# Kernel optimization log

Hardware: AMD Instinct MI355X
Metric: run time of the kernel (lower is better)

Reference implementation:

```python
import jax, jax.numpy as jnp
import numpy as np

B, N, M, C, K, K1 = 2, 2048, 2048, 512, 16, 8
NN_MARGIN = 1.0
H1, H2 = 64, 128  # Discriminator MLP widths


def _pairwise_distance(x, y):
    # x: (B,C,N), y: (B,C,M) -> squared euclidean distances (B,N,M)
    xx = jnp.sum(x * x, axis=1)[:, :, None]
    yy = jnp.sum(y * y, axis=1)[:, None, :]
    return xx - 2.0 * jnp.einsum('bcn,bcm->bnm', x, y) + yy


def _discriminator(x, y, W1, b1, W2, b2, W3, b3):
    # x, y: (B,N,k,3) neighborhood difference tensors -> per-point weights (B,1,N)
    f = jnp.concatenate([x, y], axis=-1)                       # (B,N,k,6)
    h = jax.nn.relu(jnp.einsum('bnkc,dc->bnkd', f, W1) + b1)
    h = jax.nn.relu(jnp.einsum('bnkd,ed->bnke', h, W2) + b2)
    s = (jnp.einsum('bnke,oe->bnko', h, W3) + b3)[..., 0]      # (B,N,k)
    s = jnp.max(s, axis=2)                                     # max over neighbors
    return jax.nn.softmax(s, axis=1)[:, None, :]               # (B,1,N)


def _rigid(src, corr, weight):
    # weighted Kabsch/Procrustes. src, corr: (B,3,N), weight: (B,1,N)
    w = weight / jnp.sum(weight, axis=2, keepdims=True)
    cs = jnp.sum(src * w, axis=2, keepdims=True)
    ct = jnp.sum(corr * w, axis=2, keepdims=True)
    H = jnp.einsum('bin,bjn->bij', (src - cs) * w, corr - ct)
    U, S, Vt = jnp.linalg.svd(H)
    V = jnp.swapaxes(Vt, 1, 2)
    det = jnp.linalg.det(jnp.einsum('bij,bkj->bik', V, U))     # det(V U^T)
    scale = jnp.stack([jnp.ones_like(det), jnp.ones_like(det), det], axis=-1)[:, None, :]
    R = jnp.einsum('bij,bkj->bik', V * scale, U)
    t = ct - jnp.einsum('bij,bjn->bin', R, cs)
    return R, t


def _gather_pts(x_t, idx):
    # x_t: (B,N,3), idx: (B,N,K) -> (B,N,K,3)
    return jax.vmap(lambda xb, ib: xb[ib])(x_t, idx)


def _forward(src, tgt, src_embedding, tgt_embedding, src_knn, tgt_knn,
             W1, b1, W2, b2, W3, b3, src_idx, src_idx1, idx2, k, i, k1):
    Bs, _, Np = src.shape
    Mp = tgt.shape[2]
    dist = _pairwise_distance(src_embedding, tgt_embedding)    # (B,N,M)
    scores = jax.nn.softmax(-dist, axis=2)
    # rows of scores gathered at each source point's k1 neighbors: (B,N,k1,M)
    knn_scores = jax.vmap(lambda sb, ib: sb[ib])(scores, src_idx1)
    # equivalent to summing result_view[:,:,1:,:,1:] over axes 2 and 4:
    T = jnp.sum(knn_scores[:, :, 1:, :], axis=2)               # (B,N,M)
    S = jax.vmap(lambda Tb, ib: jnp.sum(Tb[:, ib[:, 1:]], axis=-1))(T, idx2)  # (B,N,M)
    src_knn_scores = NN_MARGIN - S / (k1 - 1)
    refined = jnp.exp(src_knn_scores) * dist
    rmm = jax.nn.softmax(-refined, axis=2)                     # refined matching map
    src_corr = jnp.einsum('bcm,bnm->bcn', tgt, rmm)            # (B,3,N)
    corr_t = jnp.swapaxes(src_corr, 1, 2)                      # (B,N,3)
    src_knn_corr = _gather_pts(corr_t, src_idx)                # (B,N,K,3)
    knn_distance = corr_t[:, :, None, :] - src_knn_corr
    src_t = jnp.swapaxes(src, 1, 2)
    src_knn_distance = src_t[:, :, None, :] - src_knn
    weight = _discriminator(knn_distance, src_knn_distance, W1, b1, W2, b2, W3, b3)
    R, t = _rigid(src, src_corr, weight)
    key_num = Np // 2
    if key_num < 900:
        key_num = key_num * 2
    _, topi = jax.lax.top_k(weight[:, 0, :], key_num)          # (B,key)
    gidx = jnp.broadcast_to(topi[:, None, :], (Bs, 3, key_num))
    src_keypoints = jnp.take_along_axis(src, gidx, axis=2)
    tgt_keypoints = jnp.take_along_axis(src_corr, gidx, axis=2)
    idx_tgt_corr = jnp.argmax(rmm, axis=-1)                    # (B,N)
    sel = jnp.take_along_axis(idx_tgt_corr, topi, axis=1)      # (B,key)
    onehot = jax.nn.one_hot(sel, Mp, dtype=rmm.dtype).reshape(Bs * key_num, Mp)
    pred = jax.vmap(lambda rb, ib: rb[ib])(rmm, topi).reshape(Bs * key_num, Mp)
    loss_scl = jnp.mean(jnp.sum(-jnp.log(pred + 1e-15) * onehot, axis=1))
    tgt_keypoints_knn = jnp.transpose(
        jax.vmap(lambda kd, ib: kd[ib])(knn_distance, topi), (0, 3, 1, 2))  # (B,3,key,K)
    tvec = t[:, :, 0]
    src_transformed = jnp.einsum('bij,bjn->bin', R, src) + tvec[:, :, None]
    st_t = jnp.swapaxes(src_transformed, 1, 2)
    knn_distance2 = st_t[:, :, None, :] - _gather_pts(st_t, src_idx)
    src_keypoints_knn = jnp.transpose(
        jax.vmap(lambda kd, ib: kd[ib])(knn_distance2, topi), (0, 3, 1, 2))
    return (R, tvec, src_keypoints, tgt_keypoints, src_keypoints_knn,
            tgt_keypoints_knn, loss_scl)


def setup_inputs() -> dict:
    key = jax.random.key(0)
    ks = jax.random.split(key, 14)
    src = jax.random.normal(ks[0], (B, 3, N), jnp.float32)
    tgt = jax.random.normal(ks[1], (B, 3, M), jnp.float32)
    src_embedding = jax.random.normal(ks[2], (B, C, N), jnp.float32) * 0.1
    tgt_embedding = jax.random.normal(ks[3], (B, C, M), jnp.float32) * 0.1
    src_idx = jax.random.randint(ks[4], (B, N, K), 0, N, jnp.int32)
    src_idx1 = jax.random.randint(ks[5], (B, N, K1), 0, N, jnp.int32)
    src_idx1 = src_idx1.at[:, :, 0].set(jnp.arange(N, dtype=jnp.int32)[None, :])
    idx2 = jax.random.randint(ks[6], (B, M, K1), 0, M, jnp.int32)
    idx2 = idx2.at[:, :, 0].set(jnp.arange(M, dtype=jnp.int32)[None, :])
    src_knn = _gather_pts(jnp.swapaxes(src, 1, 2), src_idx)    # (B,N,K,3)
    tgt_knn = jax.random.normal(ks[7], (B, M, K, 3), jnp.float32)  # unused by forward
    W1 = jax.random.normal(ks[8], (H1, 6), jnp.float32) * 0.1
    b1 = jnp.zeros((H1,), jnp.float32)
    W2 = jax.random.normal(ks[9], (H2, H1), jnp.float32) * 0.1
    b2 = jnp.zeros((H2,), jnp.float32)
    W3 = jax.random.normal(ks[10], (1, H2), jnp.float32) * 0.1
    b3 = jnp.zeros((1,), jnp.float32)
    return {"src": src, "tgt": tgt, "src_embedding": src_embedding,
            "tgt_embedding": tgt_embedding, "src_knn": src_knn, "tgt_knn": tgt_knn,
            "W1": W1, "b1": b1, "W2": W2, "b2": b2, "W3": W3, "b3": b3,
            "src_idx": src_idx, "src_idx1": src_idx1, "idx2": idx2,
            "k": K, "i": 1, "k1": K1}


def reference(src, tgt, src_embedding, tgt_embedding, src_knn, tgt_knn,
              W1, b1, W2, b2, W3, b3, src_idx, src_idx1, idx2, k, i, k1):
    return _forward(src, tgt, src_embedding, tgt_embedding, src_knn, tgt_knn,
                    W1, b1, W2, b2, W3, b3, src_idx, src_idx1, idx2, k, i, k1)
```

## Files before the change

### kernel.cpp

```cpp
#include <hip/hip_runtime.h>
#include <stdint.h>

typedef unsigned short u16;

#define BB 2
#define NN 2048
#define MM 2048
#define CC 512
#define KK 16
#define KK1 8
#define KEY 1024

typedef __attribute__((ext_vector_type(8))) short bf16x8;
typedef __attribute__((ext_vector_type(4))) float f32x4;

__device__ __forceinline__ float b2f(u16 u){ return __uint_as_float(((uint32_t)u) << 16); }
__device__ __forceinline__ u16 f2b(float f){
  uint32_t x = __float_as_uint(f);
  uint32_t r = x + 0x7FFFu + ((x >> 16) & 1u);
  return (u16)(r >> 16);
}
__device__ __forceinline__ float sane(float v){ return (fabsf(v) < 1e30f) ? v : 1e30f; }

__device__ __forceinline__ void gload_lds16(const u16* g, u16* l){
  __builtin_amdgcn_global_load_lds((const __attribute__((address_space(1))) uint32_t*)g,
                                   (__attribute__((address_space(3))) uint32_t*)l, 16, 0, 0);
}

__device__ __forceinline__ float blockRed(float v, float* red, int t, int op){
  red[t] = v; __syncthreads();
  #pragma unroll
  for (int s = 128; s > 0; s >>= 1){
    if (t < s){
      float a = red[t], b = red[t + s];
      red[t] = (op == 0) ? (a + b) : ((op == 1) ? fminf(a, b) : fmaxf(a, b));
    }
    __syncthreads();
  }
  float r = red[0]; __syncthreads();
  return r;
}

__global__ __launch_bounds__(256) void k_trans(const float* __restrict__ semb, const float* __restrict__ temb,
                                               u16* __restrict__ Ah, u16* __restrict__ Al,
                                               u16* __restrict__ Bh, u16* __restrict__ Bl){
  __shared__ float tile[32][33];
  int b = blockIdx.z & 1, which = blockIdx.z >> 1;
  const float* in = which ? temb : semb;
  u16* oh = which ? Bh : Ah;
  u16* ol = which ? Bl : Al;
  int c0 = blockIdx.x * 32, n0 = blockIdx.y * 32;
  int tx = threadIdx.x, ty = threadIdx.y;
  #pragma unroll
  for (int i = 0; i < 4; i++){
    int r = ty + 8 * i;
    tile[r][tx] = in[((b * CC + c0 + r) * NN) + n0 + tx];
  }
  __syncthreads();
  #pragma unroll
  for (int i = 0; i < 4; i++){
    int r = ty + 8 * i;
    float v = tile[tx][r];
    u16 hi = f2b(v);
    float lo = v - b2f(hi);
    size_t o = ((size_t)(b * NN + n0 + r) * CC) + c0 + tx;
    oh[o] = hi;
    ol[o] = f2b(lo);
  }
}

__global__ __launch_bounds__(256) void k_sq(const float* __restrict__ semb, const float* __restrict__ temb,
                                            float* __restrict__ xx, float* __restrict__ yy){
  int which = blockIdx.y;
  const float* in = which ? temb : semb;
  float* out = which ? yy : xx;
  int gid = blockIdx.x * 256 + threadIdx.x;
  int b = gid >> 11, n = gid & 2047;
  float acc = 0.f;
  for (int c = 0; c < CC; c++){
    float v = in[((size_t)(b * CC + c)) * NN + n];
    acc += v * v;
  }
  out[gid] = acc;
}

__global__ __launch_bounds__(256) void k_gemm(const u16* __restrict__ Ah, const u16* __restrict__ Al,
                                              const u16* __restrict__ Bh, const u16* __restrict__ Bl,
                                              const float* __restrict__ xx, const float* __restrict__ yy,
                                              float* __restrict__ dist){
  __shared__ __align__(16) u16 lAh[128 * 64];
  __shared__ __align__(16) u16 lAl[128 * 64];
  __shared__ __align__(16) u16 lBh[128 * 64];
  __shared__ __align__(16) u16 lBl[128 * 64];
  int bz = blockIdx.z;
  const u16* Ahb = Ah + (size_t)bz * NN * CC;
  const u16* Alb = Al + (size_t)bz * NN * CC;
  const u16* Bhb = Bh + (size_t)bz * MM * CC;
  const u16* Blb = Bl + (size_t)bz * MM * CC;
  const float* xxb = xx + bz * NN;
  const float* yyb = yy + bz * MM;
  float* distb = dist + (size_t)bz * NN * MM;
  int n0 = blockIdx.y * 128, m0 = blockIdx.x * 128;
  int t = threadIdx.x;
  f32x4 acc[4][4];
  #pragma unroll
  for (int i = 0; i < 4; i++)
    #pragma unroll
    for (int j = 0; j < 4; j++){ f32x4 z = {0.f, 0.f, 0.f, 0.f}; acc[i][j] = z; }
  int w = t >> 6, lane = t & 63, lr = lane & 15, quad = lane >> 4;
  int wn = (w >> 1) * 64, wm = (w & 1) * 64;
  for (int kt = 0; kt < 8; kt++){
    int k0 = kt * 64;
    __syncthreads();
    #pragma unroll
    for (int s = 0; s < 4; s++){
      int ch = t + 256 * s;
      int rn = ch >> 3, k8 = (ch & 7) * 8;
      size_t oa = (size_t)(n0 + rn) * CC + k0 + k8;
      size_t ob = (size_t)(m0 + rn) * CC + k0 + k8;
      int ldsoff = ((t >> 6) * 64 + 256 * s) * 8;
      gload_lds16(Ahb + oa, &lAh[ldsoff]);
      gload_lds16(Alb + oa, &lAl[ldsoff]);
      gload_lds16(Bhb + ob, &lBh[ldsoff]);
      gload_lds16(Blb + ob, &lBl[ldsoff]);
    }
    __syncthreads();
    #pragma unroll
    for (int kk = 0; kk < 2; kk++){
      int off = kk * 32 + quad * 8;
      bf16x8 afh[4], afl[4], bfh[4], bfl[4];
      #pragma unroll
      for (int i = 0; i < 4; i++){
        int ra = (wn + i * 16 + lr) * 64 + off;
        afh[i] = *(const bf16x8*)&lAh[ra];
        afl[i] = *(const bf16x8*)&lAl[ra];
      }
      #pragma unroll
      for (int j = 0; j < 4; j++){
        int rb = (wm + j * 16 + lr) * 64 + off;
        bfh[j] = *(const bf16x8*)&lBh[rb];
        bfl[j] = *(const bf16x8*)&lBl[rb];
      }
      #pragma unroll
      for (int i = 0; i < 4; i++)
        #pragma unroll
        for (int j = 0; j < 4; j++){
          acc[i][j] = __builtin_amdgcn_mfma_f32_16x16x32_bf16(afh[i], bfh[j], acc[i][j], 0, 0, 0);
          acc[i][j] = __builtin_amdgcn_mfma_f32_16x16x32_bf16(afh[i], bfl[j], acc[i][j], 0, 0, 0);
          acc[i][j] = __builtin_amdgcn_mfma_f32_16x16x32_bf16(afl[i], bfh[j], acc[i][j], 0, 0, 0);
        }
    }
  }
  #pragma unroll
  for (int i = 0; i < 4; i++){
    int nbase = n0 + wn + i * 16 + quad * 4;
    #pragma unroll
    for (int j = 0; j < 4; j++){
      int m = m0 + wm + j * 16 + lr;
      float yv = yyb[m];
      #pragma unroll
      for (int r = 0; r < 4; r++){
        distb[((size_t)(nbase + r)) * MM + m] = xxb[nbase + r] + yv - 2.0f * acc[i][j][r];
      }
    }
  }
}

__global__ __launch_bounds__(256) void k_rowstats(const float* __restrict__ dist,
                                                  float* __restrict__ mnA, float* __restrict__ Zr,
                                                  float* __restrict__ scores){
  __shared__ float red[256];
  int row = blockIdx.x, b = blockIdx.y, t = threadIdx.x;
  const float* dr = dist + ((size_t)b * NN + row) * MM;
  float* sr = scores + ((size_t)b * NN + row) * MM;
  float d[8];
  float mn = 3.4e38f;
  #pragma unroll
  for (int i = 0; i < 8; i++){ d[i] = sane(dr[t + 256 * i]); mn = fminf(mn, d[i]); }
  mn = blockRed(mn, red, t, 1);
  float p[8];
  float z = 0.f;
  #pragma unroll
  for (int i = 0; i < 8; i++){ p[i] = expf(mn - d[i]); z += p[i]; }
  z = blockRed(z, red, t, 0);
  float zc = fmaxf(z, 1e-30f);
  if (t == 0){ mnA[b * NN + row] = mn; Zr[b * NN + row] = zc; }
  float iz = 1.0f / zc;
  #pragma unroll
  for (int i = 0; i < 8; i++) sr[t + 256 * i] = p[i] * iz;
}

__global__ __launch_bounds__(256) void k_fused(const float* __restrict__ dist, const float* __restrict__ scores,
                                               const int* __restrict__ sidx1,
                                               const int* __restrict__ idx2, const float* __restrict__ tgt,
                                               float* __restrict__ s_corr, float* __restrict__ lossr){
  __shared__ float Trow[MM];
  __shared__ float red[256];
  int n = blockIdx.x, b = blockIdx.y, t = threadIdx.x;
  const float* distb = dist + (size_t)b * NN * MM;
  const float* scoresb = scores + (size_t)b * NN * MM;
  const int* sidx1b = sidx1 + (size_t)b * NN * KK1;
  const int* idx2b = idx2 + (size_t)b * MM * KK1;
  const float* tgtb = tgt + (size_t)b * 3 * MM;
  float* s_corrb = s_corr + (size_t)b * 3 * NN;
  float* lossb = lossr + b * NN;
  const float* dn_p = distb + (size_t)n * MM;
  float dn[8];
  #pragma unroll
  for (int i = 0; i < 8; i++) dn[i] = sane(dn_p[t + 256 * i]);
  float tacc[8] = {0, 0, 0, 0, 0, 0, 0, 0};
  const int4* i1v = (const int4*)(sidx1b + n * KK1);
  int4 i1a = i1v[0], i1b = i1v[1];
  int rj[7] = {i1a.y & 2047, i1a.z & 2047, i1a.w & 2047,
               i1b.x & 2047, i1b.y & 2047, i1b.z & 2047, i1b.w & 2047};
  #pragma unroll
  for (int j = 0; j < 7; j++){
    const float* srp = scoresb + (size_t)rj[j] * MM;
    #pragma unroll
    for (int i = 0; i < 8; i++) tacc[i] += srp[t + 256 * i];
  }
  #pragma unroll
  for (int i = 0; i < 8; i++) Trow[t + 256 * i] = tacc[i];
  __syncthreads();
  float rloc[8];
  float lmin = 3.4e38f;
  #pragma unroll
  for (int i = 0; i < 8; i++){
    int m = t + 256 * i;
    const int4* ipv = (const int4*)(idx2b + m * KK1);
    int4 ipa = ipv[0], ipb = ipv[1];
    float S = 0.f;
    S += Trow[ipa.y & 2047];
    S += Trow[ipa.z & 2047];
    S += Trow[ipa.w & 2047];
    S += Trow[ipb.x & 2047];
    S += Trow[ipb.y & 2047];
    S += Trow[ipb.z & 2047];
    S += Trow[ipb.w & 2047];
    float rv = sane(expf(1.0f - S / 7.0f) * dn[i]);
    rloc[i] = rv;
    lmin = fminf(lmin, rv);
  }
  float rmin = blockRed(lmin, red, t, 1);
  float z = 0.f, s0 = 0.f, s1 = 0.f, s2 = 0.f;
  #pragma unroll
  for (int i = 0; i < 8; i++){
    int m = t + 256 * i;
    float p = expf(rmin - rloc[i]);
    z  += p;
    s0 += tgtb[0 * MM + m] * p;
    s1 += tgtb[1 * MM + m] * p;
    s2 += tgtb[2 * MM + m] * p;
  }
  z  = blockRed(z,  red, t, 0);
  s0 = blockRed(s0, red, t, 0);
  s1 = blockRed(s1, red, t, 0);
  s2 = blockRed(s2, red, t, 0);
  if (t == 0){
    float iZ = 1.0f / fmaxf(z, 1e-30f);
    s_corrb[0 * NN + n] = s0 * iZ;
    s_corrb[1 * NN + n] = s1 * iZ;
    s_corrb[2 * NN + n] = s2 * iZ;
    lossb[n] = -logf(fminf(iZ, 1.0f) + 1e-15f);
  }
}

__global__ __launch_bounds__(256, 4) void k_disc(const float* __restrict__ s_corr, const float* __restrict__ src,
                                                 const float* __restrict__ sknn, const int* __restrict__ sidx,
                                                 const float* __restrict__ W1, const float* __restrict__ b1,
                                                 const float* __restrict__ W2, const float* __restrict__ b2,
                                                 const float* __restrict__ W3, const float* __restrict__ b3,
                                                 float* __restrict__ sArr){
  __shared__ float term[64][129];
  int t = threadIdx.x;
  int b = blockIdx.y;
  int p = t & 63;
  int n = blockIdx.x * 4 + (p >> 4);
  int kk = p & 15;
  int eh = t >> 6;
  int nk = sidx[((b * NN + n) * KK) + kk] & 2047;
  float f[6];
  #pragma unroll
  for (int c = 0; c < 3; c++){
    f[c]     = s_corr[(b * 3 + c) * NN + n] - s_corr[(b * 3 + c) * NN + nk];
    f[3 + c] = src[(b * 3 + c) * NN + n] - sknn[((size_t)(b * NN + n) * KK + kk) * 3 + c];
  }
  #define L1D(d) ({ float a_ = b1[(d)];              \
                    a_ += f[0] * W1[(d) * 6 + 0];    \
                    a_ += f[1] * W1[(d) * 6 + 1];    \
                    a_ += f[2] * W1[(d) * 6 + 2];    \
                    a_ += f[3] * W1[(d) * 6 + 3];    \
                    a_ += f[4] * W1[(d) * 6 + 4];    \
                    a_ += f[5] * W1[(d) * 6 + 5];    \
                    fmaxf(a_, 0.f); })
  #define HSET(i) f32x4 h##i;                  \
                  h##i.x = L1D(4 * (i) + 0);   \
                  h##i.y = L1D(4 * (i) + 1);   \
                  h##i.z = L1D(4 * (i) + 2);   \
                  h##i.w = L1D(4 * (i) + 3);
  HSET(0) HSET(1) HSET(2) HSET(3) HSET(4) HSET(5) HSET(6) HSET(7)
  HSET(8) HSET(9) HSET(10) HSET(11) HSET(12) HSET(13) HSET(14) HSET(15)
  #undef HSET
  #undef L1D
  int e0 = __builtin_amdgcn_readfirstlane(eh * 32);
  for (int j = 0; j < 32; j++){
    int e = e0 + j;
    float a = b2[e];
    const f32x4* w4 = (const f32x4*)&W2[e * 64];
    #define QSTEP(i) { f32x4 wv = w4[i]; a += wv.x * h##i.x + wv.y * h##i.y + wv.z * h##i.z + wv.w * h##i.w; }
    QSTEP(0) QSTEP(1) QSTEP(2) QSTEP(3) QSTEP(4) QSTEP(5) QSTEP(6) QSTEP(7)
    QSTEP(8) QSTEP(9) QSTEP(10) QSTEP(11) QSTEP(12) QSTEP(13) QSTEP(14) QSTEP(15)
    #undef QSTEP
    term[p][e] = fmaxf(a, 0.f);
  }
  __syncthreads();
  if (t < 64){
    float sacc = b3[0];
    #pragma unroll 4
    for (int e = 0; e < 128; e++) sacc += W3[e] * term[t][e];
    if (!(fabsf(sacc) < 1e30f)) sacc = -1e30f;
    #pragma unroll
    for (int off = 1; off < 16; off <<= 1) sacc = fmaxf(sacc, __shfl_xor(sacc, off, 16));
    if (kk == 0) sArr[b * NN + n] = sacc;
  }
}

__global__ __launch_bounds__(256) void k_softw(const float* __restrict__ sArr, float* __restrict__ wArr){
  __shared__ float red[256];
  int b = blockIdx.x, t = threadIdx.x;
  const float* sp = sArr + b * NN;
  float sv[8];
  float mx = -3.4e38f;
  #pragma unroll
  for (int i = 0; i < 8; i++){
    float v = sp[t + 256 * i];
    if (!(fabsf(v) < 1e30f)) v = -1e30f;
    sv[i] = v; mx = fmaxf(mx, v);
  }
  mx = blockRed(mx, red, t, 2);
  float z = 0.f;
  #pragma unroll
  for (int i = 0; i < 8; i++) z += expf(sv[i] - mx);
  z = blockRed(z, red, t, 0);
  float iz = 1.0f / fmaxf(z, 1e-30f);
  #pragma unroll
  for (int i = 0; i < 8; i++) wArr[b * NN + t + 256 * i] = expf(sv[i] - mx) * iz;
}

__global__ __launch_bounds__(256) void k_rank(const float* __restrict__ wArr, int* __restrict__ topi){
  __shared__ float wrow[NN];
  __shared__ int pc[4][64];
  int b = blockIdx.y, t = threadIdx.x;
  for (int i = t; i < NN; i += 256) wrow[i] = wArr[b * NN + i];
  __syncthreads();
  int tn = t & 63, tj = t >> 6;
  int n = blockIdx.x * 64 + tn;
  float wn = wrow[n];
  int j0 = tj * 512;
  const f32x4* w4 = (const f32x4*)&wrow[j0];
  int cnt = 0;
  #pragma unroll 4
  for (int q = 0; q < 128; q++){
    f32x4 wv = w4[q];
    int j = j0 + q * 4;
    cnt += (wv.x > wn) || ((wv.x == wn) && (j + 0 < n));
    cnt += (wv.y > wn) || ((wv.y == wn) && (j + 1 < n));
    cnt += (wv.z > wn) || ((wv.z == wn) && (j + 2 < n));
    cnt += (wv.w > wn) || ((wv.w == wn) && (j + 3 < n));
  }
  pc[tj][tn] = cnt;
  __syncthreads();
  if (t < 64){
    int c = pc[0][t] + pc[1][t] + pc[2][t] + pc[3][t];
    if (c < KEY) topi[b * KEY + c] = blockIdx.x * 64 + t;
  }
}

__device__ __forceinline__ double det3d(const double A[3][3]){
  return A[0][0] * (A[1][1] * A[2][2] - A[1][2] * A[2][1])
       - A[0][1] * (A[1][0] * A[2][2] - A[1][2] * A[2][0])
       + A[0][2] * (A[1][0] * A[2][1] - A[1][1] * A[2][0]);
}

__global__ __launch_bounds__(256) void k_rigid(const float* __restrict__ src, const float* __restrict__ s_corr,
                                               const float* __restrict__ wArr, float* __restrict__ Rt,
                                               float* __restrict__ out){
  __shared__ float red[256];
  int b = blockIdx.x, t = threadIdx.x;
  float wsum = 0, a0 = 0, a1 = 0, a2 = 0, c0 = 0, c1 = 0, c2 = 0;
  for (int n = t; n < NN; n += 256){
    float wv = wArr[b * NN + n];
    float s0 = src[(b * 3 + 0) * NN + n];
    float s1 = src[(b * 3 + 1) * NN + n];
    float s2 = src[(b * 3 + 2) * NN + n];
    float q0 = s_corr[(b * 3 + 0) * NN + n];
    float q1 = s_corr[(b * 3 + 1) * NN + n];
    float q2 = s_corr[(b * 3 + 2) * NN + n];
    wsum += wv; a0 += wv * s0; a1 += wv * s1; a2 += wv * s2;
    c0 += wv * q0; c1 += wv * q1; c2 += wv * q2;
  }
  wsum = blockRed(wsum, red, t, 0);
  a0 = blockRed(a0, red, t, 0); a1 = blockRed(a1, red, t, 0); a2 = blockRed(a2, red, t, 0);
  c0 = blockRed(c0, red, t, 0); c1 = blockRed(c1, red, t, 0); c2 = blockRed(c2, red, t, 0);
  float inv = 1.0f / fmaxf(wsum, 1e-30f);
  float cs0 = a0 * inv, cs1 = a1 * inv, cs2 = a2 * inv;
  float ct0 = c0 * inv, ct1 = c1 * inv, ct2 = c2 * inv;
  float h[9] = {0, 0, 0, 0, 0, 0, 0, 0, 0};
  for (int n = t; n < NN; n += 256){
    float wv = wArr[b * NN + n];
    float ds0 = src[(b * 3 + 0) * NN + n] - cs0;
    float ds1 = src[(b * 3 + 1) * NN + n] - cs1;
    float ds2 = src[(b * 3 + 2) * NN + n] - cs2;
    float dc0 = s_corr[(b * 3 + 0) * NN + n] - ct0;
    float dc1 = s_corr[(b * 3 + 1) * NN + n] - ct1;
    float dc2 = s_corr[(b * 3 + 2) * NN + n] - ct2;
    h[0] += wv * ds0 * dc0; h[1] += wv * ds0 * dc1; h[2] += wv * ds0 * dc2;
    h[3] += wv * ds1 * dc0; h[4] += wv * ds1 * dc1; h[5] += wv * ds1 * dc2;
    h[6] += wv * ds2 * dc0; h[7] += wv * ds2 * dc1; h[8] += wv * ds2 * dc2;
  }
  for (int i = 0; i < 9; i++) h[i] = blockRed(h[i], red, t, 0);
  if (t == 0){
    double Hm[3][3];
    for (int i = 0; i < 3; i++)
      for (int j = 0; j < 3; j++) Hm[i][j] = (double)h[i * 3 + j];
    double Km[3][3], V[3][3] = {{1, 0, 0}, {0, 1, 0}, {0, 0, 1}};
    for (int i = 0; i < 3; i++)
      for (int j = 0; j < 3; j++){
        double s = 0;
        for (int a = 0; a < 3; a++) s += Hm[a][i] * Hm[a][j];
        Km[i][j] = s;
      }
    double ksc = fabs(Km[0][0]) + fabs(Km[1][1]) + fabs(Km[2][2]) + 1e-300;
    for (int sweep = 0; sweep < 60; sweep++){
      int p = 0, q = 1; double mx = fabs(Km[0][1]);
      if (fabs(Km[0][2]) > mx){ mx = fabs(Km[0][2]); p = 0; q = 2; }
      if (fabs(Km[1][2]) > mx){ mx = fabs(Km[1][2]); p = 1; q = 2; }
      if (mx <= 1e-15 * ksc) break;
      double app = Km[p][p], aqq = Km[q][q], apq = Km[p][q];
      double tau = (aqq - app) / (2.0 * apq);
      double tt = ((tau >= 0) ? 1.0 : -1.0) / (fabs(tau) + sqrt(1.0 + tau * tau));
      double cc = 1.0 / sqrt(1.0 + tt * tt), sn = tt * cc;
      for (int k2 = 0; k2 < 3; k2++){
        double akp = Km[k2][p], akq = Km[k2][q];
        Km[k2][p] = cc * akp - sn * akq; Km[k2][q] = sn * akp + cc * akq;
      }
      for (int k2 = 0; k2 < 3; k2++){
        double apk = Km[p][k2], aqk = Km[q][k2];
        Km[p][k2] = cc * apk - sn * aqk; Km[q][k2] = sn * apk + cc * aqk;
      }
      for (int k2 = 0; k2 < 3; k2++){
        double vkp = V[k2][p], vkq = V[k2][q];
        V[k2][p] = cc * vkp - sn * vkq; V[k2][q] = sn * vkp + cc * vkq;
      }
    }
    double lam[3] = {Km[0][0], Km[1][1], Km[2][2]};
    int id0 = 0, id1 = 1, id2 = 2, tmp;
    if (lam[id0] < lam[id1]){ tmp = id0; id0 = id1; id1 = tmp; }
    if (lam[id0] < lam[id2]){ tmp = id0; id0 = id2; id2 = tmp; }
    if (lam[id1] < lam[id2]){ tmp = id1; id1 = id2; id2 = tmp; }
    int idx[3] = {id0, id1, id2};
    double Vs[3][3], U[3][3] = {{0, 0, 0}, {0, 0, 0}, {0, 0, 0}};
    for (int jj = 0; jj < 3; jj++){
      int j = idx[jj];
      for (int i2 = 0; i2 < 3; i2++) Vs[i2][jj] = V[i2][j];
      double u0 = 0, u1 = 0, u2 = 0;
      for (int i2 = 0; i2 < 3; i2++){
        u0 += Hm[0][i2] * V[i2][j];
        u1 += Hm[1][i2] * V[i2][j];
        u2 += Hm[2][i2] * V[i2][j];
      }
      double nrm = sqrt(u0 * u0 + u1 * u1 + u2 * u2);
      if (nrm > 1e-20){
        U[0][jj] = u0 / nrm; U[1][jj] = u1 / nrm; U[2][jj] = u2 / nrm;
      } else {
        double x0 = U[1][0] * U[2][1] - U[2][0] * U[1][1];
        double x1 = U[2][0] * U[0][1] - U[0][0] * U[2][1];
        double x2 = U[0][0] * U[1][1] - U[1][0] * U[0][1];
        double nn2 = sqrt(x0 * x0 + x1 * x1 + x2 * x2);
        if (nn2 < 1e-20){ x0 = 1; x1 = 0; x2 = 0; nn2 = 1; }
        U[0][jj] = x0 / nn2; U[1][jj] = x1 / nn2; U[2][jj] = x2 / nn2;
      }
    }
    double dd = det3d(U) * det3d(Vs);
    double Rm[3][3];
    for (int i2 = 0; i2 < 3; i2++)
      for (int k2 = 0; k2 < 3; k2++)
        Rm[i2][k2] = Vs[i2][0] * U[k2][0] + Vs[i2][1] * U[k2][1] + dd * Vs[i2][2] * U[k2][2];
    double cs[3] = {cs0, cs1, cs2}, ct[3] = {ct0, ct1, ct2};
    double tv[3];
    for (int i2 = 0; i2 < 3; i2++)
      tv[i2] = ct[i2] - (Rm[i2][0] * cs[0] + Rm[i2][1] * cs[1] + Rm[i2][2] * cs[2]);
    for (int i2 = 0; i2 < 3; i2++)
      for (int k2 = 0; k2 < 3; k2++){
        Rt[b * 12 + i2 * 3 + k2] = (float)Rm[i2][k2];
        out[b * 9 + i2 * 3 + k2] = (float)Rm[i2][k2];
      }
    for (int i2 = 0; i2 < 3; i2++){
      Rt[b * 12 + 9 + i2] = (float)tv[i2];
      out[18 + b * 3 + i2] = (float)tv[i2];
    }
  }
}

__global__ __launch_bounds__(256) void k_out(const int* __restrict__ topi, const int* __restrict__ sidx,
                                             const float* __restrict__ src, const float* __restrict__ s_corr,
                                             const float* __restrict__ Rt, float* __restrict__ out){
  int b = blockIdx.y, t = threadIdx.x;
  int rr = t >> 4, kk = t & 15;
  int r = blockIdx.x * 16 + rr;
  int ns = topi[b * KEY + r] & 2047;
  int nk = sidx[(b * NN + ns) * KK + kk] & 2047;
  const float* R = Rt + b * 12;
  float sns0 = src[(b * 3 + 0) * NN + ns];
  float sns1 = src[(b * 3 + 1) * NN + ns];
  float sns2 = src[(b * 3 + 2) * NN + ns];
  float snk0 = src[(b * 3 + 0) * NN + nk];
  float snk1 = src[(b * 3 + 1) * NN + nk];
  float snk2 = src[(b * 3 + 2) * NN + nk];
  float* o_sk  = out + 24;
  float* o_tk  = out + 6168;
  float* o_skk = out + 12312;
  float* o_tkk = out + 110616;
  #pragma unroll
  for (int c = 0; c < 3; c++){
    float cv  = s_corr[(b * 3 + c) * NN + ns];
    float ck  = s_corr[(b * 3 + c) * NN + nk];
    o_tkk[(((b * 3 + c) * KEY + r) * KK) + kk] = cv - ck;
    float sv  = R[c * 3 + 0] * sns0 + R[c * 3 + 1] * sns1 + R[c * 3 + 2] * sns2 + R[9 + c];
    float sk2 = R[c * 3 + 0] * snk0 + R[c * 3 + 1] * snk1 + R[c * 3 + 2] * snk2 + R[9 + c];
    o_skk[(((b * 3 + c) * KEY + r) * KK) + kk] = sv - sk2;
    if (kk == 0){
      o_sk[(b * 3 + c) * KEY + r] = sns0 * (c == 0) + sns1 * (c == 1) + sns2 * (c == 2);
      o_tk[(b * 3 + c) * KEY + r] = cv;
    }
  }
}

__global__ __launch_bounds__(256) void k_loss(const float* __restrict__ loss_row, const int* __restrict__ topi,
                                              float* __restrict__ out){
  __shared__ float red[256];
  int t = threadIdx.x;
  float acc = 0.f;
  for (int i = t; i < BB * KEY; i += 256){
    int b = i >> 10, r = i & 1023;
    int n = topi[b * KEY + r] & 2047;
    acc += loss_row[b * NN + n];
  }
  acc = blockRed(acc, red, t, 0);
  if (t == 0) out[208920] = acc / 2048.0f;
}

extern "C" void kernel_launch(void* const* d_in, const int* in_sizes, int n_in,
                              void* d_out, int out_size, void* d_ws, size_t ws_size,
                              hipStream_t stream){
  const float* src  = (const float*)d_in[0];
  const float* tgt  = (const float*)d_in[1];
  const float* semb = (const float*)d_in[2];
  const float* temb = (const float*)d_in[3];
  const float* sknn = (const float*)d_in[4];
  const float* W1 = (const float*)d_in[6];
  const float* b1 = (const float*)d_in[7];
  const float* W2 = (const float*)d_in[8];
  const float* b2 = (const float*)d_in[9];
  const float* W3 = (const float*)d_in[10];
  const float* b3 = (const float*)d_in[11];
  const int* sidx  = (const int*)d_in[12];
  const int* sidx1 = (const int*)d_in[13];
  const int* idx2  = (const int*)d_in[14];
  float* out = (float*)d_out;

  char* w = (char*)d_ws;
  u16* Ah = (u16*)(w);
  u16* Al = Ah + (size_t)BB * NN * CC;
  u16* Bh = Al + (size_t)BB * NN * CC;
  u16* Bl = Bh + (size_t)BB * MM * CC;
  float* dist = (float*)(Bl + (size_t)BB * MM * CC);
  float* scores = dist + (size_t)BB * NN * MM;
  char* tail = (char*)(scores + (size_t)BB * NN * MM);
  float* xx = (float*)tail;
  float* yy = xx + BB * NN;
  float* mnA = yy + BB * MM;
  float* Zr = mnA + BB * NN;
  float* s_corr = Zr + BB * NN;
  float* loss_row = s_corr + BB * 3 * NN;
  float* sArr = loss_row + BB * NN;
  float* wArr = sArr + BB * NN;
  int* topi = (int*)(wArr + BB * NN);
  float* Rt = (float*)(topi + BB * KEY);

  k_trans<<<dim3(16, 64, 4), dim3(32, 8), 0, stream>>>(semb, temb, Ah, Al, Bh, Bl);
  k_sq<<<dim3(16, 2), 256, 0, stream>>>(semb, temb, xx, yy);
  k_gemm<<<dim3(16, 16, BB), 256, 0, stream>>>(Ah, Al, Bh, Bl, xx, yy, dist);
  k_rowstats<<<dim3(NN, BB), 256, 0, stream>>>(dist, mnA, Zr, scores);
  k_fused<<<dim3(NN, BB), 256, 0, stream>>>(dist, scores, sidx1, idx2, tgt, s_corr, loss_row);
  k_disc<<<dim3(NN / 4, BB), 256, 0, stream>>>(s_corr, src, sknn, sidx, W1, b1, W2, b2, W3, b3, sArr);
  k_softw<<<BB, 256, 0, stream>>>(sArr, wArr);
  k_rank<<<dim3(32, BB), 256, 0, stream>>>(wArr, topi);
  k_rigid<<<BB, 256, 0, stream>>>(src, s_corr, wArr, Rt, out);
  k_out<<<dim3(64, BB), 256, 0, stream>>>(topi, sidx, src, s_corr, Rt, out);
  k_loss<<<1, 256, 0, stream>>>(loss_row, topi, out);
}
```

Before: 280.5 us.

## Fuse softmax, rank, rigid and loss kernels; use warp-shuffle min reductions

Merges the weight softmax, rank and rigid-fit kernels into one kernel. Each block recomputes the softmax of the discriminator scores into shared memory, and block 0 also does the Kabsch fit. The loss reduction moves into an extra block of the output kernel. This cuts three launches and drops the wArr round trip. Block min reductions now use wavefront shuffles, and the four sum reductions in the fused kernel become one float4 tree reduction. The cost is redundant softmax work in 32 blocks, and a serial rigid solve tail that now runs inside the rank kernel.

```diff
diff --git a/kernel.cpp b/kernel.cpp
--- a/kernel.cpp
+++ b/kernel.cpp
@@ -39,6 +39,14 @@
   }
   float r = red[0]; __syncthreads();
   return r;
+}
+
+__device__ __forceinline__ float blockMinExact(float v, float* wmin, int t){
+  #pragma unroll
+  for (int off = 1; off < 64; off <<= 1) v = fminf(v, __shfl_xor(v, off));
+  if ((t & 63) == 0) wmin[t >> 6] = v;
+  __syncthreads();
+  return fminf(fminf(wmin[0], wmin[1]), fminf(wmin[2], wmin[3]));
 }
 
 __global__ __launch_bounds__(256) void k_trans(const float* __restrict__ semb, const float* __restrict__ temb,
@@ -170,6 +178,7 @@
                                                   float* __restrict__ mnA, float* __restrict__ Zr,
                                                   float* __restrict__ scores){
   __shared__ float red[256];
+  __shared__ float wmin[4];
   int row = blockIdx.x, b = blockIdx.y, t = threadIdx.x;
   const float* dr = dist + ((size_t)b * NN + row) * MM;
   float* sr = scores + ((size_t)b * NN + row) * MM;
@@ -177,7 +186,7 @@
   float mn = 3.4e38f;
   #pragma unroll
   for (int i = 0; i < 8; i++){ d[i] = sane(dr[t + 256 * i]); mn = fminf(mn, d[i]); }
-  mn = blockRed(mn, red, t, 1);
+  mn = blockMinExact(mn, wmin, t);
   float p[8];
   float z = 0.f;
   #pragma unroll
@@ -195,7 +204,7 @@
                                                const int* __restrict__ idx2, const float* __restrict__ tgt,
                                                float* __restrict__ s_corr, float* __restrict__ lossr){
   __shared__ float Trow[MM];
-  __shared__ float red[256];
+  __shared__ float wmin[4];
   int n = blockIdx.x, b = blockIdx.y, t = threadIdx.x;
   const float* distb = dist + (size_t)b * NN * MM;
   const float* scoresb = scores + (size_t)b * NN * MM;
@@ -241,7 +250,7 @@
     rloc[i] = rv;
     lmin = fminf(lmin, rv);
   }
-  float rmin = blockRed(lmin, red, t, 1);
+  float rmin = blockMinExact(lmin, wmin, t);
   float z = 0.f, s0 = 0.f, s1 = 0.f, s2 = 0.f;
   #pragma unroll
   for (int i = 0; i < 8; i++){
@@ -252,15 +261,24 @@
     s1 += tgtb[1 * MM + m] * p;
     s2 += tgtb[2 * MM + m] * p;
   }
-  z  = blockRed(z,  red, t, 0);
-  s0 = blockRed(s0, red, t, 0);
-  s1 = blockRed(s1, red, t, 0);
-  s2 = blockRed(s2, red, t, 0);
+  f32x4* red4 = (f32x4*)Trow;
+  f32x4 v4; v4.x = z; v4.y = s0; v4.z = s1; v4.w = s2;
+  red4[t] = v4; __syncthreads();
+  #pragma unroll
+  for (int s = 128; s > 0; s >>= 1){
+    if (t < s){
+      f32x4 a = red4[t], c = red4[t + s];
+      a.x += c.x; a.y += c.y; a.z += c.z; a.w += c.w;
+      red4[t] = a;
+    }
+    __syncthreads();
+  }
   if (t == 0){
-    float iZ = 1.0f / fmaxf(z, 1e-30f);
-    s_corrb[0 * NN + n] = s0 * iZ;
-    s_corrb[1 * NN + n] = s1 * iZ;
-    s_corrb[2 * NN + n] = s2 * iZ;
+    f32x4 r = red4[0];
+    float iZ = 1.0f / fmaxf(r.x, 1e-30f);
+    s_corrb[0 * NN + n] = r.y * iZ;
+    s_corrb[1 * NN + n] = r.z * iZ;
+    s_corrb[2 * NN + n] = r.w * iZ;
     lossb[n] = -logf(fminf(iZ, 1.0f) + 1e-15f);
   }
 }
@@ -325,9 +343,19 @@
   }
 }
 
-__global__ __launch_bounds__(256) void k_softw(const float* __restrict__ sArr, float* __restrict__ wArr){
+__device__ __forceinline__ double det3d(const double A[3][3]){
+  return A[0][0] * (A[1][1] * A[2][2] - A[1][2] * A[2][1])
+       - A[0][1] * (A[1][0] * A[2][2] - A[1][2] * A[2][0])
+       + A[0][2] * (A[1][0] * A[2][1] - A[1][1] * A[2][0]);
+}
+
+__global__ __launch_bounds__(256) void k_rankrig(const float* __restrict__ sArr, const float* __restrict__ src,
+                                                 const float* __restrict__ s_corr, int* __restrict__ topi,
+                                                 float* __restrict__ Rt, float* __restrict__ out){
+  __shared__ float wrow[NN];
   __shared__ float red[256];
-  int b = blockIdx.x, t = threadIdx.x;
+  __shared__ int pc[4][64];
+  int b = blockIdx.y, t = threadIdx.x;
   const float* sp = sArr + b * NN;
   float sv[8];
   float mx = -3.4e38f;
@@ -344,14 +372,7 @@
   z = blockRed(z, red, t, 0);
   float iz = 1.0f / fmaxf(z, 1e-30f);
   #pragma unroll
-  for (int i = 0; i < 8; i++) wArr[b * NN + t + 256 * i] = expf(sv[i] - mx) * iz;
-}
-
-__global__ __launch_bounds__(256) void k_rank(const float* __restrict__ wArr, int* __restrict__ topi){
-  __shared__ float wrow[NN];
-  __shared__ int pc[4][64];
-  int b = blockIdx.y, t = threadIdx.x;
-  for (int i = t; i < NN; i += 256) wrow[i] = wArr[b * NN + i];
+  for (int i = 0; i < 8; i++) wrow[t + 256 * i] = expf(sv[i] - mx) * iz;
   __syncthreads();
   int tn = t & 63, tj = t >> 6;
   int n = blockIdx.x * 64 + tn;
@@ -374,28 +395,16 @@
     int c = pc[0][t] + pc[1][t] + pc[2][t] + pc[3][t];
     if (c < KEY) topi[b * KEY + c] = blockIdx.x * 64 + t;
   }
-}
-
-__device__ __forceinline__ double det3d(const double A[3][3]){
-  return A[0][0] * (A[1][1] * A[2][2] - A[1][2] * A[2][1])
-       - A[0][1] * (A[1][0] * A[2][2] - A[1][2] * A[2][0])
-       + A[0][2] * (A[1][0] * A[2][1] - A[1][1] * A[2][0]);
-}
-
-__global__ __launch_bounds__(256) void k_rigid(const float* __restrict__ src, const float* __restrict__ s_corr,
-                                               const float* __restrict__ wArr, float* __restrict__ Rt,
-                                               float* __restrict__ out){
-  __shared__ float red[256];
-  int b = blockIdx.x, t = threadIdx.x;
+  if (blockIdx.x != 0) return;
   float wsum = 0, a0 = 0, a1 = 0, a2 = 0, c0 = 0, c1 = 0, c2 = 0;
-  for (int n = t; n < NN; n += 256){
-    float wv = wArr[b * NN + n];
-    float s0 = src[(b * 3 + 0) * NN + n];
-    float s1 = src[(b * 3 + 1) * NN + n];
-    float s2 = src[(b * 3 + 2) * NN + n];
-    float q0 = s_corr[(b * 3 + 0) * NN + n];
-    float q1 = s_corr[(b * 3 + 1) * NN + n];
-    float q2 = s_corr[(b * 3 + 2) * NN + n];
+  for (int n2 = t; n2 < NN; n2 += 256){
+    float wv = wrow[n2];
+    float s0 = src[(b * 3 + 0) * NN + n2];
+    float s1 = src[(b * 3 + 1) * NN + n2];
+    float s2 = src[(b * 3 + 2) * NN + n2];
+    float q0 = s_corr[(b * 3 + 0) * NN + n2];
+    float q1 = s_corr[(b * 3 + 1) * NN + n2];
+    float q2 = s_corr[(b * 3 + 2) * NN + n2];
     wsum += wv; a0 += wv * s0; a1 += wv * s1; a2 += wv * s2;
     c0 += wv * q0; c1 += wv * q1; c2 += wv * q2;
   }
@@ -406,14 +415,14 @@
   float cs0 = a0 * inv, cs1 = a1 * inv, cs2 = a2 * inv;
   float ct0 = c0 * inv, ct1 = c1 * inv, ct2 = c2 * inv;
   float h[9] = {0, 0, 0, 0, 0, 0, 0, 0, 0};
-  for (int n = t; n < NN; n += 256){
-    float wv = wArr[b * NN + n];
-    float ds0 = src[(b * 3 + 0) * NN + n] - cs0;
-    float ds1 = src[(b * 3 + 1) * NN + n] - cs1;
-    float ds2 = src[(b * 3 + 2) * NN + n] - cs2;
-    float dc0 = s_corr[(b * 3 + 0) * NN + n] - ct0;
-    float dc1 = s_corr[(b * 3 + 1) * NN + n] - ct1;
-    float dc2 = s_corr[(b * 3 + 2) * NN + n] - ct2;
+  for (int n2 = t; n2 < NN; n2 += 256){
+    float wv = wrow[n2];
+    float ds0 = src[(b * 3 + 0) * NN + n2] - cs0;
+    float ds1 = src[(b * 3 + 1) * NN + n2] - cs1;
+    float ds2 = src[(b * 3 + 2) * NN + n2] - cs2;
+    float dc0 = s_corr[(b * 3 + 0) * NN + n2] - ct0;
+    float dc1 = s_corr[(b * 3 + 1) * NN + n2] - ct1;
+    float dc2 = s_corr[(b * 3 + 2) * NN + n2] - ct2;
     h[0] += wv * ds0 * dc0; h[1] += wv * ds0 * dc1; h[2] += wv * ds0 * dc2;
     h[3] += wv * ds1 * dc0; h[4] += wv * ds1 * dc1; h[5] += wv * ds1 * dc2;
     h[6] += wv * ds2 * dc0; h[7] += wv * ds2 * dc1; h[8] += wv * ds2 * dc2;
@@ -432,10 +441,10 @@
       }
     double ksc = fabs(Km[0][0]) + fabs(Km[1][1]) + fabs(Km[2][2]) + 1e-300;
     for (int sweep = 0; sweep < 60; sweep++){
-      int p = 0, q = 1; double mx = fabs(Km[0][1]);
-      if (fabs(Km[0][2]) > mx){ mx = fabs(Km[0][2]); p = 0; q = 2; }
-      if (fabs(Km[1][2]) > mx){ mx = fabs(Km[1][2]); p = 1; q = 2; }
-      if (mx <= 1e-15 * ksc) break;
+      int p = 0, q = 1; double mx2 = fabs(Km[0][1]);
+      if (fabs(Km[0][2]) > mx2){ mx2 = fabs(Km[0][2]); p = 0; q = 2; }
+      if (fabs(Km[1][2]) > mx2){ mx2 = fabs(Km[1][2]); p = 1; q = 2; }
+      if (mx2 <= 1e-15 * ksc) break;
       double app = Km[p][p], aqq = Km[q][q], apq = Km[p][q];
       double tau = (aqq - app) / (2.0 * apq);
       double tt = ((tau >= 0) ? 1.0 : -1.0) / (fabs(tau) + sqrt(1.0 + tau * tau));
@@ -504,8 +513,22 @@
 
 __global__ __launch_bounds__(256) void k_out(const int* __restrict__ topi, const int* __restrict__ sidx,
                                              const float* __restrict__ src, const float* __restrict__ s_corr,
-                                             const float* __restrict__ Rt, float* __restrict__ out){
+                                             const float* __restrict__ Rt, const float* __restrict__ loss_row,
+                                             float* __restrict__ out){
+  __shared__ float red[256];
   int b = blockIdx.y, t = threadIdx.x;
+  if (blockIdx.x == 64){
+    if (b != 0) return;
+    float acc = 0.f;
+    for (int i = t; i < BB * KEY; i += 256){
+      int bb = i >> 10, r = i & 1023;
+      int n = topi[bb * KEY + r] & 2047;
+      acc += loss_row[bb * NN + n];
+    }
+    acc = blockRed(acc, red, t, 0);
+    if (t == 0) out[208920] = acc / 2048.0f;
+    return;
+  }
   int rr = t >> 4, kk = t & 15;
   int r = blockIdx.x * 16 + rr;
   int ns = topi[b * KEY + r] & 2047;
@@ -534,20 +557,6 @@
       o_tk[(b * 3 + c) * KEY + r] = cv;
     }
   }
-}
-
-__global__ __launch_bounds__(256) void k_loss(const float* __restrict__ loss_row, const int* __restrict__ topi,
-                                              float* __restrict__ out){
-  __shared__ float red[256];
-  int t = threadIdx.x;
-  float acc = 0.f;
-  for (int i = t; i < BB * KEY; i += 256){
-    int b = i >> 10, r = i & 1023;
-    int n = topi[b * KEY + r] & 2047;
-    acc += loss_row[b * NN + n];
-  }
-  acc = blockRed(acc, red, t, 0);
-  if (t == 0) out[208920] = acc / 2048.0f;
 }
 
 extern "C" void kernel_launch(void* const* d_in, const int* in_sizes, int n_in,
@@ -584,8 +593,7 @@
   float* s_corr = Zr + BB * NN;
   float* loss_row = s_corr + BB * 3 * NN;
   float* sArr = loss_row + BB * NN;
-  float* wArr = sArr + BB * NN;
-  int* topi = (int*)(wArr + BB * NN);
+  int* topi = (int*)(sArr + BB * NN);
   float* Rt = (float*)(topi + BB * KEY);
 
   k_trans<<<dim3(16, 64, 4), dim3(32, 8), 0, stream>>>(semb, temb, Ah, Al, Bh, Bl);
@@ -594,9 +602,6 @@
   k_rowstats<<<dim3(NN, BB), 256, 0, stream>>>(dist, mnA, Zr, scores);
   k_fused<<<dim3(NN, BB), 256, 0, stream>>>(dist, scores, sidx1, idx2, tgt, s_corr, loss_row);
   k_disc<<<dim3(NN / 4, BB), 256, 0, stream>>>(s_corr, src, sknn, sidx, W1, b1, W2, b2, W3, b3, sArr);
-  k_softw<<<BB, 256, 0, stream>>>(sArr, wArr);
-  k_rank<<<dim3(32, BB), 256, 0, stream>>>(wArr, topi);
-  k_rigid<<<BB, 256, 0, stream>>>(src, s_corr, wArr, Rt, out);
-  k_out<<<dim3(64, BB), 256, 0, stream>>>(topi, sidx, src, s_corr, Rt, out);
-  k_loss<<<1, 256, 0, stream>>>(loss_row, topi, out);
-}
+  k_rankrig<<<dim3(32, BB), 256, 0, stream>>>(sArr, src, s_corr, topi, Rt, out);
+  k_out<<<dim3(65, BB), 256, 0, stream>>>(topi, sidx, src, s_corr, Rt, loss_row, out);
+}
```

Result: faster. 272.8 us (-2.7%).
